# Kernel tuning notes

Measured on AMD Instinct MI355X. Metric: run time of the kernel, lower is better.

The kernel has to match this reference:

```python
import math
import jax, jax.numpy as jnp
import numpy as np

T, D, H = 2048, 2048, 16
C = D // H
EPS = 1e-6


def _rope_tables(c, t):
    inv_freq = 1.0 / (10000.0 ** (jnp.arange(0, c, 2, dtype=jnp.float32) / c))
    freqs = jnp.arange(t, dtype=jnp.float32)[:, None] * inv_freq[None, :]  # (T, C/2)
    return jnp.sin(freqs), jnp.cos(freqs)


def _rotate_every_two(x):
    x1 = x[..., ::2]
    x2 = x[..., 1::2]
    return jnp.stack((-x2, x1), axis=-1).reshape(x.shape)


def _apply_rope(x_htc, sin, cos):
    # sin/cos: (T, C/2) -> repeat each freq twice along channel -> (1, T, C)
    sin = jnp.repeat(sin, 2, axis=-1)[None]
    cos = jnp.repeat(cos, 2, axis=-1)[None]
    return x_htc * cos + _rotate_every_two(x_htc) * sin


def _layernorm(x, w):
    mu = jnp.mean(x, axis=-1, keepdims=True)
    var = jnp.var(x, axis=-1, keepdims=True)
    return (x - mu) / jnp.sqrt(var + EPS) * w


def setup_inputs() -> dict:
    key = jax.random.key(0)
    ks = jax.random.split(key, 4)
    x = jax.random.normal(ks[0], (T, D), dtype=jnp.float32)
    W_attn = jax.random.normal(ks[1], (3 * D, D), dtype=jnp.float32) * 0.02
    b_attn = jnp.zeros((3 * D,), dtype=jnp.float32)
    W_proj = jax.random.normal(ks[2], (D, D), dtype=jnp.float32) * 0.02
    b_proj = jnp.zeros((D,), dtype=jnp.float32)
    q_ln_w = jnp.ones((C,), dtype=jnp.float32)
    k_ln_w = jnp.ones((C,), dtype=jnp.float32)
    return {"x": x, "W_attn": W_attn, "b_attn": b_attn, "W_proj": W_proj,
            "b_proj": b_proj, "q_ln_w": q_ln_w, "k_ln_w": k_ln_w}


def reference(x, W_attn, b_attn, W_proj, b_proj, q_ln_w, k_ln_w):
    t, d = x.shape
    qkv = x @ W_attn.T + b_attn                      # (T, 3D)
    q, k, v = jnp.split(qkv, 3, axis=-1)
    q = q.reshape(t, H, C).transpose(1, 0, 2)        # (H, T, C)
    k = k.reshape(t, H, C).transpose(1, 0, 2)
    v = v.reshape(t, H, C).transpose(1, 0, 2)
    q = _layernorm(q, q_ln_w)
    k = _layernorm(k, k_ln_w)
    sin, cos = _rope_tables(C, t)
    q = _apply_rope(q, sin, cos)
    k = _apply_rope(k, sin, cos)
    a = jnp.einsum("htc,hsc->hts", q, k)             # (H, T, T)
    causal = jnp.tril(jnp.ones((1, t, t))) == 0
    a = jnp.where(causal, float("-inf"), a)
    scaling = math.sqrt(C)                            # q_ln active
    a = jax.nn.softmax(a.astype(jnp.float32) / scaling, axis=-1).astype(x.dtype)
    out = jnp.einsum("hts,hsc->htc", a, v)           # (H, T, C)
    out = out.transpose(1, 0, 2).reshape(t, d)       # (T, D)
    return out @ W_proj.T + b_proj
```

## Files before the change

### kernel.cpp

```cpp
#include <hip/hip_runtime.h>
#include <hip/hip_bf16.h>
#include <math.h>

#define T_DIM 2048
#define D_DIM 2048
#define H_DIM 16
#define C_DIM 128

typedef __bf16 bf16;
typedef __attribute__((ext_vector_type(8))) __bf16 bf16x8;
typedef __attribute__((ext_vector_type(4))) __bf16 bf16x4;
typedef __attribute__((ext_vector_type(2))) __bf16 bf16x2;
typedef __attribute__((ext_vector_type(4))) float f32x4;

__device__ __forceinline__ void gload_lds16(const void* g, void* l) {
  __builtin_amdgcn_global_load_lds((__attribute__((address_space(1))) void*)g,
                                   (__attribute__((address_space(3))) void*)l,
                                   16, 0, 0);
}

__global__ __launch_bounds__(256) void cvt3(
    const float* __restrict__ x, const float* __restrict__ wa, const float* __restrict__ wp,
    bf16* __restrict__ xo, bf16* __restrict__ wao, bf16* __restrict__ wpo)
{
  const int NX = 1048576, NA = 3145728;
  int i = blockIdx.x * 256 + threadIdx.x;
  for (; i < 5242880; i += 2048 * 256) {
    const float* s; bf16* d; int off;
    if (i < NX)            { s = x;  d = xo;  off = i; }
    else if (i < NX + NA)  { s = wa; d = wao; off = i - NX; }
    else                   { s = wp; d = wpo; off = i - NX - NA; }
    float4 v = reinterpret_cast<const float4*>(s)[off];
    bf16x4 o;
    o[0] = (bf16)v.x; o[1] = (bf16)v.y; o[2] = (bf16)v.z; o[3] = (bf16)v.w;
    reinterpret_cast<bf16x4*>(d)[off] = o;
  }
}

__global__ __launch_bounds__(512, 2) void gemm384_bt_bias(
    const bf16* __restrict__ A, const bf16* __restrict__ B,
    const float* __restrict__ bias, float* __restrict__ C,
    int M, int N, int K)
{
  __shared__ __align__(16) bf16 Asl[2][128 * 64];
  __shared__ __align__(16) bf16 Bsl[2][384 * 64];
  const int tid = threadIdx.x;
  const int lane = tid & 63;
  const int wv = tid >> 6;
  const int g = lane >> 4, r16 = lane & 15;
  const int wm4 = wv >> 1;
  const int wn2 = wv & 1;

  int bid = blockIdx.x;
  int bid2 = (bid & 7) * 32 + (bid >> 3);
  const int ntn = N / 384;
  const int bn = bid2 % ntn, bm = bid2 / ntn;

  const size_t Abase = (size_t)(bm * 128) * K;
  const size_t Bbase = (size_t)(bn * 384) * K;

  f32x4 acc[4][2][3] = {};
  bf16x8 a[2][2], b[3][2];

  auto stageA = [&](int bb, int t) {
#pragma unroll
    for (int i = 0; i < 2; ++i) {
      int c = i * 512 + tid;
      int r = c >> 3, p = c & 7, j = p ^ (r & 7);
      gload_lds16(A + Abase + (size_t)r * K + t * 64 + j * 8,
                  (char*)&Asl[bb][0] + (size_t)c * 16);
    }
  };
  auto stageB = [&](int bb, int u, int t) {
#pragma unroll
    for (int i = 0; i < 2; ++i) {
      int c = i * 512 + tid;
      int r = c >> 3, p = c & 7, j = p ^ (r & 7);
      gload_lds16(B + Bbase + (size_t)(u * 128 + r) * K + t * 64 + j * 8,
                  (char*)&Bsl[bb][0] + u * 16384 + (size_t)c * 16);
    }
  };
  auto readA = [&](int bufi) {
#pragma unroll
    for (int R = 0; R < 2; ++R) {
      int ar = wm4 * 32 + R * 16 + r16;
#pragma unroll
      for (int ks = 0; ks < 2; ++ks)
        a[R][ks] = *reinterpret_cast<const bf16x8*>(
            &Asl[bufi][ar * 64 + (((ks * 4 + g) ^ (ar & 7)) << 3)]);
    }
  };
  auto readB = [&](int bufi, int q) {
#pragma unroll
    for (int F = 0; F < 3; ++F) {
      int br = q * 96 + wn2 * 48 + F * 16 + r16;
#pragma unroll
      for (int ks = 0; ks < 2; ++ks)
        b[F][ks] = *reinterpret_cast<const bf16x8*>(
            &Bsl[bufi][br * 64 + (((ks * 4 + g) ^ (br & 7)) << 3)]);
    }
  };
  auto mfma12 = [&](f32x4 (&cq)[2][3]) {
    __builtin_amdgcn_s_setprio(1);
#pragma unroll
    for (int ks = 0; ks < 2; ++ks)
#pragma unroll
      for (int R = 0; R < 2; ++R)
#pragma unroll
        for (int F = 0; F < 3; ++F)
          cq[R][F] = __builtin_amdgcn_mfma_f32_16x16x32_bf16(a[R][ks], b[F][ks], cq[R][F], 0, 0, 0);
    __builtin_amdgcn_s_setprio(0);
  };

#define VMSYNC(VM)                                                \
  asm volatile("s_waitcnt vmcnt(" #VM ")" ::: "memory");          \
  __builtin_amdgcn_s_barrier();                                   \
  asm volatile("s_waitcnt lgkmcnt(0)" ::: "memory");              \
  __builtin_amdgcn_sched_barrier(0);
#define BARSYNC()                                                 \
  __builtin_amdgcn_s_barrier();                                   \
  asm volatile("s_waitcnt lgkmcnt(0)" ::: "memory");              \
  __builtin_amdgcn_sched_barrier(0);

  stageA(0, 0); stageB(0, 0, 0); stageB(0, 1, 0); stageB(0, 2, 0);
  asm volatile("s_waitcnt vmcnt(4)" ::: "memory");
  __builtin_amdgcn_s_barrier();

  const int NT = K >> 6;
  for (int t = 0; t < NT; ++t) {
    const int cb = t & 1, nb = cb ^ 1;
    const bool pf = (t + 1 < NT);
    readA(cb);
    readB(cb, 0);
    if (pf) stageA(nb, t + 1);
    VMSYNC(4)
    mfma12(acc[0]);
    __builtin_amdgcn_s_barrier();
    readB(cb, 1);
    if (pf) stageB(nb, 0, t + 1);
    VMSYNC(4)
    mfma12(acc[1]);
    __builtin_amdgcn_s_barrier();
    readB(cb, 2);
    if (pf) stageB(nb, 1, t + 1);
    BARSYNC()
    mfma12(acc[2]);
    __builtin_amdgcn_s_barrier();
    readB(cb, 3);
    if (pf) stageB(nb, 2, t + 1);
    VMSYNC(4)
    mfma12(acc[3]);
    __builtin_amdgcn_s_barrier();
  }
#undef VMSYNC
#undef BARSYNC

#pragma unroll
  for (int q = 0; q < 4; ++q)
#pragma unroll
    for (int R = 0; R < 2; ++R)
#pragma unroll
      for (int F = 0; F < 3; ++F) {
        int row0 = bm * 128 + wm4 * 32 + R * 16 + g * 4;
        int col  = bn * 384 + q * 96 + wn2 * 48 + F * 16 + r16;
        float bv = bias[col];
#pragma unroll
        for (int rr = 0; rr < 4; ++rr)
          C[(size_t)(row0 + rr) * N + col] = acc[q][R][F][rr] + bv;
      }
}

__global__ __launch_bounds__(256) void gemm_bt_bias(
    const bf16* __restrict__ A, const bf16* __restrict__ B,
    const float* __restrict__ bias, float* __restrict__ C,
    int M, int N, int K)
{
  __shared__ __align__(16) bf16 As[2][128 * 32];
  __shared__ __align__(16) bf16 Bs[2][128 * 32];
  const int tid = threadIdx.x;
  const int lane = tid & 63;
  const int w = tid >> 6;
  const int wm = (w >> 1) * 64, wn = (w & 1) * 64;
  const int g = lane >> 4;
  const int r16 = lane & 15;
  const int bm = blockIdx.y, bn = blockIdx.x;

  f32x4 acc[4][4] = {};

  const size_t Abase = (size_t)(bm * 128) * K;
  const size_t Bbase = (size_t)(bn * 128) * K;

  auto stage = [&](int bb, int k0) {
#pragma unroll
    for (int c = 0; c < 2; ++c) {
      int e = c * 256 + tid;
      int row = e >> 2, col = (e & 3) * 8;
      gload_lds16(A + Abase + (size_t)row * K + k0 + col, (char*)&As[bb][0] + (size_t)e * 16);
      gload_lds16(B + Bbase + (size_t)row * K + k0 + col, (char*)&Bs[bb][0] + (size_t)e * 16);
    }
  };

  stage(0, 0);
  __syncthreads();

  for (int k0 = 0; k0 < K; k0 += 32) {
    const int cur = (k0 >> 5) & 1;
    if (k0 + 32 < K) stage(cur ^ 1, k0 + 32);
    bf16x8 a[4], b[4];
#pragma unroll
    for (int m = 0; m < 4; ++m)
      a[m] = *reinterpret_cast<const bf16x8*>(&As[cur][(wm + m * 16 + r16) * 32 + g * 8]);
#pragma unroll
    for (int n = 0; n < 4; ++n)
      b[n] = *reinterpret_cast<const bf16x8*>(&Bs[cur][(wn + n * 16 + r16) * 32 + g * 8]);
    __builtin_amdgcn_s_setprio(1);
#pragma unroll
    for (int m = 0; m < 4; ++m)
#pragma unroll
      for (int n = 0; n < 4; ++n)
        acc[m][n] = __builtin_amdgcn_mfma_f32_16x16x32_bf16(a[m], b[n], acc[m][n], 0, 0, 0);
    __builtin_amdgcn_s_setprio(0);
    __syncthreads();
  }

#pragma unroll
  for (int m = 0; m < 4; ++m) {
    int row0 = bm * 128 + wm + m * 16 + g * 4;
#pragma unroll
    for (int n = 0; n < 4; ++n) {
      int col = bn * 128 + wn + n * 16 + r16;
      float bv = bias[col];
#pragma unroll
      for (int rr = 0; rr < 4; ++rr)
        C[(size_t)(row0 + rr) * N + col] = acc[m][n][rr] + bv;
    }
  }
}

__global__ __launch_bounds__(256) void lnrope_vt_kernel(
    const float* __restrict__ qkv, const float* __restrict__ qw,
    const float* __restrict__ kw, bf16* __restrict__ qo, bf16* __restrict__ ko,
    bf16* __restrict__ vt)
{
  __shared__ bf16 tile[32][33];
  const int tid = threadIdx.x;
  if (blockIdx.x < 8192) {
    const int lane = tid & 63;
    const int wid = blockIdx.x * 4 + (tid >> 6);
    const int h = wid >> 11;
    const int t = wid & (T_DIM - 1);
    const int c0 = lane * 2;

    float inv_freq = exp2f(-13.287712379549449f * (float)c0 * (1.0f / 128.0f));
    float fr = (float)t * inv_freq;
    float sn = sinf(fr), cs = cosf(fr);
    const float scaleq = 0.08838834764831845f;

#pragma unroll
    for (int which = 0; which < 2; ++which) {
      const float* base = qkv + (size_t)t * (3 * D_DIM) + which * D_DIM + h * C_DIM;
      float2 v = *reinterpret_cast<const float2*>(base + c0);
      float s = v.x + v.y;
#pragma unroll
      for (int m = 32; m; m >>= 1) s += __shfl_xor(s, m);
      float mu = s * (1.0f / 128.0f);
      float d0 = v.x - mu, d1 = v.y - mu;
      float ss = d0 * d0 + d1 * d1;
#pragma unroll
      for (int m = 32; m; m >>= 1) ss += __shfl_xor(ss, m);
      float rstd = rsqrtf(ss * (1.0f / 128.0f) + 1e-6f);
      const float* wgt = which ? kw : qw;
      float x0 = d0 * rstd * wgt[c0], x1 = d1 * rstd * wgt[c0 + 1];
      float o0 = x0 * cs - x1 * sn;
      float o1 = x1 * cs + x0 * sn;
      if (!which) { o0 *= scaleq; o1 *= scaleq; }
      bf16* out = (which ? ko : qo) + ((size_t)h * T_DIM + t) * C_DIM + c0;
      bf16x2 ob; ob[0] = (bf16)o0; ob[1] = (bf16)o1;
      *reinterpret_cast<bf16x2*>(out) = ob;
    }
  } else {
    const int vb = blockIdx.x - 8192;
    const int t0 = (vb & 63) * 32;
    const int c0 = ((vb >> 6) & 3) * 32;
    const int h = vb >> 8;
    const int tx = tid & 31, ty = tid >> 5;
#pragma unroll
    for (int i = 0; i < 4; ++i) {
      int t = t0 + ty + i * 8;
      tile[ty + i * 8][tx] =
          (bf16)qkv[(size_t)t * (3 * D_DIM) + 2 * D_DIM + h * C_DIM + c0 + tx];
    }
    __syncthreads();
#pragma unroll
    for (int i = 0; i < 4; ++i) {
      int c = c0 + ty + i * 8;
      vt[((size_t)h * C_DIM + c) * T_DIM + t0 + tx] = tile[tx][ty + i * 8];
    }
  }
}

__global__ __launch_bounds__(256, 4) void attn_kernel(
    const bf16* __restrict__ Q, const bf16* __restrict__ K,
    const bf16* __restrict__ VT, bf16* __restrict__ AO,
    float* __restrict__ U, float* __restrict__ ML)
{
  __shared__ __align__(16) bf16 Ks[2][32 * 128];
  __shared__ __align__(16) bf16 Vs[2][128 * 32];
  __shared__ __align__(16) bf16 p_lds[4][16 * 32];
  const int tid = threadIdx.x;
  const int lane = tid & 63;
  const int w = tid >> 6;
  const int g = lane >> 4, r16 = lane & 15;
  const int h = blockIdx.y;
  const int b = blockIdx.x;

  int qb, kb0, kb1, sp;
  if (b < 32) { qb = 16 + (b >> 1); sp = b & 1; kb0 = sp * 32; kb1 = sp ? (2 * qb + 2) : 32; }
  else        { qb = 47 - b;        sp = -1;    kb0 = 0;       kb1 = 2 * qb + 2; }
  const int qr0 = qb * 64 + w * 16;
  const int qrow = qr0 + r16;

  const bf16* Qh = Q + (size_t)h * T_DIM * C_DIM;
  const bf16* Kh = K + (size_t)h * T_DIM * C_DIM;
  const bf16* Vh = VT + (size_t)h * C_DIM * T_DIM;

  bf16x8 qf[4];
#pragma unroll
  for (int kk = 0; kk < 4; ++kk)
    qf[kk] = *reinterpret_cast<const bf16x8*>(
        &Qh[(size_t)qrow * C_DIM + kk * 32 + g * 8]);

  float mrow = -INFINITY, lrow = 0.f;
  f32x4 o[8] = {};

  auto stage = [&](int bb, int kb) {
    const bf16* Kt = Kh + (size_t)(kb * 32) * C_DIM;
    const bf16* Vt = Vh + kb * 32;
#pragma unroll
    for (int i = 0; i < 2; ++i) {
      int e = i * 256 + tid;
      int r = e >> 4, p = e & 15, j = p ^ (r & 7);
      gload_lds16(Kt + r * C_DIM + j * 8, (char*)&Ks[bb][0] + (size_t)e * 16);
    }
#pragma unroll
    for (int i = 0; i < 2; ++i) {
      int e = i * 256 + tid;
      int r = e >> 2, p = e & 3, j = p ^ ((r >> 1) & 3);
      gload_lds16(Vt + (size_t)r * T_DIM + j * 8, (char*)&Vs[bb][0] + (size_t)e * 16);
    }
  };

  stage(0, kb0);
  __syncthreads();
  int buf = 0;

  for (int kb = kb0; kb < kb1; ++kb) {
    if (kb + 1 < kb1) stage(buf ^ 1, kb + 1);

    f32x4 sacc[2] = {};
    __builtin_amdgcn_s_setprio(1);
#pragma unroll
    for (int n = 0; n < 2; ++n) {
      int kr = n * 16 + r16;
      const bf16* kbase = &Ks[buf][kr << 7];
#pragma unroll
      for (int kk = 0; kk < 4; ++kk) {
        bf16x8 kf = *reinterpret_cast<const bf16x8*>(
            kbase + (((kk * 4 + g) ^ (kr & 7)) << 3));
        sacc[n] = __builtin_amdgcn_mfma_f32_16x16x32_bf16(kf, qf[kk], sacc[n], 0, 0, 0);
      }
    }
    __builtin_amdgcn_s_setprio(0);
    if (kb * 32 + 31 > qr0) {
#pragma unroll
      for (int n = 0; n < 2; ++n)
#pragma unroll
        for (int rr = 0; rr < 4; ++rr)
          if (kb * 32 + n * 16 + g * 4 + rr > qrow) sacc[n][rr] = -3.0e38f;
    }
    float mx = fmaxf(fmaxf(fmaxf(sacc[0][0], sacc[0][1]), fmaxf(sacc[0][2], sacc[0][3])),
                     fmaxf(fmaxf(sacc[1][0], sacc[1][1]), fmaxf(sacc[1][2], sacc[1][3])));
    mx = fmaxf(mx, __shfl_xor(mx, 16));
    mx = fmaxf(mx, __shfl_xor(mx, 32));
    float alpha = 1.0f;
    bool need = __any(mx > mrow + 8.0f);
    if (need) {
      float mnew = fmaxf(mrow, mx);
      alpha = __expf(mrow - mnew);
      mrow = mnew;
    }
    float ps = 0.f;
#pragma unroll
    for (int n = 0; n < 2; ++n)
#pragma unroll
      for (int rr = 0; rr < 4; ++rr) {
        float p = __expf(sacc[n][rr] - mrow);
        sacc[n][rr] = p;
        ps += p;
      }
    ps += __shfl_xor(ps, 16);
    ps += __shfl_xor(ps, 32);
    lrow = lrow * alpha + ps;
    if (need) {
#pragma unroll
      for (int nc = 0; nc < 8; ++nc)
#pragma unroll
        for (int rr = 0; rr < 4; ++rr)
          o[nc][rr] *= alpha;
    }
    {
      bf16* prow = &p_lds[w][r16 << 5];
      const int ssw = (r16 >> 1) & 3;
#pragma unroll
      for (int n = 0; n < 2; ++n) {
        bf16x4 pk;
        pk[0] = (bf16)sacc[n][0]; pk[1] = (bf16)sacc[n][1];
        pk[2] = (bf16)sacc[n][2]; pk[3] = (bf16)sacc[n][3];
        int c8 = 2 * n + (g >> 1);
        *reinterpret_cast<bf16x4*>(prow + (((c8 ^ ssw) << 3) | ((g & 1) << 2))) = pk;
      }
    }
    asm volatile("s_waitcnt lgkmcnt(0)" ::: "memory");
    __builtin_amdgcn_s_setprio(1);
    bf16x8 pf = *reinterpret_cast<const bf16x8*>(
        &p_lds[w][(r16 << 5) + ((g ^ ((r16 >> 1) & 3)) << 3)]);
#pragma unroll
    for (int nc = 0; nc < 8; ++nc) {
      int vr = nc * 16 + r16;
      bf16x8 vf = *reinterpret_cast<const bf16x8*>(
          &Vs[buf][(vr << 5) + ((g ^ ((vr >> 1) & 3)) << 3)]);
      o[nc] = __builtin_amdgcn_mfma_f32_16x16x32_bf16(vf, pf, o[nc], 0, 0, 0);
    }
    __builtin_amdgcn_s_setprio(0);
    __syncthreads();
    buf ^= 1;
  }

  if (sp < 0) {
    float inv = 1.0f / lrow;
    bf16* arow = &AO[(size_t)qrow * D_DIM + h * C_DIM + (g << 2)];
#pragma unroll
    for (int nc = 0; nc < 8; ++nc) {
      bf16x4 ob;
      ob[0] = (bf16)(o[nc][0] * inv); ob[1] = (bf16)(o[nc][1] * inv);
      ob[2] = (bf16)(o[nc][2] * inv); ob[3] = (bf16)(o[nc][3] * inv);
      *reinterpret_cast<bf16x4*>(arow + nc * 16) = ob;
    }
  } else {
    const int qi = qb - 16;
    const size_t ubase = ((size_t)(h * 16 + qi) * 2 + sp) * (64 * 128);
    const size_t mlbase = (size_t)(h * 16 + qi) * 256 + sp * 128;
    const int row = w * 16 + r16;
    float* urow = &U[ubase + (size_t)row * 128 + (g << 2)];
#pragma unroll
    for (int nc = 0; nc < 8; ++nc)
      *reinterpret_cast<f32x4*>(urow + nc * 16) = o[nc];
    if (g == 0) {
      ML[mlbase + row] = mrow;
      ML[mlbase + 64 + row] = lrow;
    }
  }
}

__global__ __launch_bounds__(256) void attn_combine(
    const float* __restrict__ U, const float* __restrict__ ML, bf16* __restrict__ AO)
{
  int idx = blockIdx.x * 256 + threadIdx.x;
  int c4 = (idx & 31) * 4;
  int r = idx >> 5;
  int trow = r & 63;
  int qi = (r >> 6) & 15;
  int h = r >> 10;

  size_t mlbase = (size_t)(h * 16 + qi) * 256;
  float m0 = ML[mlbase + trow],       l0 = ML[mlbase + 64 + trow];
  float m1 = ML[mlbase + 128 + trow], l1 = ML[mlbase + 192 + trow];
  float m = fmaxf(m0, m1);
  float a0 = __expf(m0 - m), a1 = __expf(m1 - m);
  float inv = 1.0f / (l0 * a0 + l1 * a1);

  size_t t0 = ((size_t)(h * 16 + qi) * 2) * (64 * 128) + (size_t)trow * 128 + c4;
  float4 u0 = *reinterpret_cast<const float4*>(U + t0);
  float4 u1 = *reinterpret_cast<const float4*>(U + t0 + 64 * 128);
  int t = 1024 + qi * 64 + trow;
  bf16x4 ob;
  ob[0] = (bf16)((u0.x * a0 + u1.x * a1) * inv);
  ob[1] = (bf16)((u0.y * a0 + u1.y * a1) * inv);
  ob[2] = (bf16)((u0.z * a0 + u1.z * a1) * inv);
  ob[3] = (bf16)((u0.w * a0 + u1.w * a1) * inv);
  *reinterpret_cast<bf16x4*>(&AO[(size_t)t * D_DIM + h * C_DIM + c4]) = ob;
}

extern "C" void kernel_launch(void* const* d_in, const int* in_sizes, int n_in,
                              void* d_out, int out_size, void* d_ws, size_t ws_size,
                              hipStream_t stream)
{
  const float* x      = (const float*)d_in[0];
  const float* W_attn = (const float*)d_in[1];
  const float* b_attn = (const float*)d_in[2];
  const float* W_proj = (const float*)d_in[3];
  const float* b_proj = (const float*)d_in[4];
  const float* q_ln_w = (const float*)d_in[5];
  const float* k_ln_w = (const float*)d_in[6];

  char* ws = (char*)d_ws;
  bf16*  x_bf  = (bf16*)(ws + 0);
  bf16*  wa_bf = (bf16*)(ws + 8388608);
  bf16*  wp_bf = (bf16*)(ws + 33554432);
  float* qkv   = (float*)(ws + 41943040);
  bf16*  q_bf  = (bf16*)(ws + 92274688);
  bf16*  k_bf  = (bf16*)(ws + 100663296);
  bf16*  vt    = (bf16*)(ws + 109051904);
  bf16*  ao    = (bf16*)(ws + 117440512);
  float* U  = (float*)(ws + 41943040);
  float* ML = (float*)(ws + 58720256);

  cvt3<<<2048, 256, 0, stream>>>(x, W_attn, W_proj, x_bf, wa_bf, wp_bf);

  gemm384_bt_bias<<<dim3((T_DIM / 128) * (3 * D_DIM / 384)), dim3(512), 0, stream>>>(
      x_bf, wa_bf, b_attn, qkv, T_DIM, 3 * D_DIM, D_DIM);

  lnrope_vt_kernel<<<8192 + 4096, 256, 0, stream>>>(qkv, q_ln_w, k_ln_w, q_bf, k_bf, vt);

  attn_kernel<<<dim3(48, H_DIM), 256, 0, stream>>>(q_bf, k_bf, vt, ao, U, ML);
  attn_combine<<<2048, 256, 0, stream>>>(U, ML, ao);

  gemm_bt_bias<<<dim3(D_DIM / 128, T_DIM / 128), 256, 0, stream>>>(
      ao, wp_bf, b_proj, (float*)d_out, T_DIM, D_DIM, D_DIM);
}
```

Baseline: 191.3 us.

## Remap QKV GEMM warps to 2x4 grid with register-reused A/B fragments

Changes the wave layout of the 128x384 QKV GEMM from 4x2 (32 rows each, cycling over four B column groups) to 2x4 (64 rows by 96 columns per wave). Each wave now holds two A and two B fragment sets and runs four MFMA phases over their cross products, so the LDS fragment reads per K-step drop from 4 A plus 12 B loads to 2 A plus 2 B groups. Global prefetch is regrouped into three phases with a single vmcnt(0) wait at the end of each iteration. This raises register use and gives up the finer-grained vmcnt overlap of the previous schedule.

```diff
diff --git a/kernel.cpp b/kernel.cpp
--- a/kernel.cpp
+++ b/kernel.cpp
@@ -48,8 +48,8 @@
   const int lane = tid & 63;
   const int wv = tid >> 6;
   const int g = lane >> 4, r16 = lane & 15;
-  const int wm4 = wv >> 1;
-  const int wn2 = wv & 1;
+  const int wm = wv >> 2;
+  const int wn = wv & 3;
 
   int bid = blockIdx.x;
   int bid2 = (bid & 7) * 32 + (bid >> 3);
@@ -59,8 +59,9 @@
   const size_t Abase = (size_t)(bm * 128) * K;
   const size_t Bbase = (size_t)(bn * 384) * K;
 
-  f32x4 acc[4][2][3] = {};
-  bf16x8 a[2][2], b[3][2];
+  f32x4 acc[2][2][2][3] = {};
+  bf16x8 a0[2][2], a1[2][2];
+  bf16x8 b0[3][2], b1[3][2];
 
   auto stageA = [&](int bb, int t) {
 #pragma unroll
@@ -80,27 +81,27 @@
                   (char*)&Bsl[bb][0] + u * 16384 + (size_t)c * 16);
     }
   };
-  auto readA = [&](int bufi) {
+  auto readAh = [&](bf16x8 (&dst)[2][2], int bufi, int qr) {
 #pragma unroll
     for (int R = 0; R < 2; ++R) {
-      int ar = wm4 * 32 + R * 16 + r16;
+      int ar = wm * 64 + qr * 32 + R * 16 + r16;
 #pragma unroll
       for (int ks = 0; ks < 2; ++ks)
-        a[R][ks] = *reinterpret_cast<const bf16x8*>(
+        dst[R][ks] = *reinterpret_cast<const bf16x8*>(
             &Asl[bufi][ar * 64 + (((ks * 4 + g) ^ (ar & 7)) << 3)]);
     }
   };
-  auto readB = [&](int bufi, int q) {
+  auto readBh = [&](bf16x8 (&dst)[3][2], int bufi, int qc) {
 #pragma unroll
     for (int F = 0; F < 3; ++F) {
-      int br = q * 96 + wn2 * 48 + F * 16 + r16;
+      int br = wn * 96 + qc * 48 + F * 16 + r16;
 #pragma unroll
       for (int ks = 0; ks < 2; ++ks)
-        b[F][ks] = *reinterpret_cast<const bf16x8*>(
+        dst[F][ks] = *reinterpret_cast<const bf16x8*>(
             &Bsl[bufi][br * 64 + (((ks * 4 + g) ^ (br & 7)) << 3)]);
     }
   };
-  auto mfma12 = [&](f32x4 (&cq)[2][3]) {
+  auto mfma12 = [&](f32x4 (&cq)[2][3], bf16x8 (&aa)[2][2], bf16x8 (&bb)[3][2]) {
     __builtin_amdgcn_s_setprio(1);
 #pragma unroll
     for (int ks = 0; ks < 2; ++ks)
@@ -108,66 +109,60 @@
       for (int R = 0; R < 2; ++R)
 #pragma unroll
         for (int F = 0; F < 3; ++F)
-          cq[R][F] = __builtin_amdgcn_mfma_f32_16x16x32_bf16(a[R][ks], b[F][ks], cq[R][F], 0, 0, 0);
+          cq[R][F] = __builtin_amdgcn_mfma_f32_16x16x32_bf16(aa[R][ks], bb[F][ks], cq[R][F], 0, 0, 0);
     __builtin_amdgcn_s_setprio(0);
   };
 
-#define VMSYNC(VM)                                                \
-  asm volatile("s_waitcnt vmcnt(" #VM ")" ::: "memory");          \
+#define PHASESYNC()                                               \
   __builtin_amdgcn_s_barrier();                                   \
   asm volatile("s_waitcnt lgkmcnt(0)" ::: "memory");              \
   __builtin_amdgcn_sched_barrier(0);
-#define BARSYNC()                                                 \
-  __builtin_amdgcn_s_barrier();                                   \
-  asm volatile("s_waitcnt lgkmcnt(0)" ::: "memory");              \
-  __builtin_amdgcn_sched_barrier(0);
 
   stageA(0, 0); stageB(0, 0, 0); stageB(0, 1, 0); stageB(0, 2, 0);
-  asm volatile("s_waitcnt vmcnt(4)" ::: "memory");
+  asm volatile("s_waitcnt vmcnt(0)" ::: "memory");
   __builtin_amdgcn_s_barrier();
 
   const int NT = K >> 6;
   for (int t = 0; t < NT; ++t) {
     const int cb = t & 1, nb = cb ^ 1;
     const bool pf = (t + 1 < NT);
-    readA(cb);
-    readB(cb, 0);
-    if (pf) stageA(nb, t + 1);
-    VMSYNC(4)
-    mfma12(acc[0]);
+    readAh(a0, cb, 0);
+    readBh(b0, cb, 0);
+    if (pf) { stageA(nb, t + 1); stageB(nb, 0, t + 1); }
+    PHASESYNC()
+    mfma12(acc[0][0], a0, b0);
     __builtin_amdgcn_s_barrier();
-    readB(cb, 1);
-    if (pf) stageB(nb, 0, t + 1);
-    VMSYNC(4)
-    mfma12(acc[1]);
+    readBh(b1, cb, 1);
+    if (pf) stageB(nb, 1, t + 1);
+    PHASESYNC()
+    mfma12(acc[0][1], a0, b1);
     __builtin_amdgcn_s_barrier();
-    readB(cb, 2);
-    if (pf) stageB(nb, 1, t + 1);
-    BARSYNC()
-    mfma12(acc[2]);
+    readAh(a1, cb, 1);
+    if (pf) stageB(nb, 2, t + 1);
+    PHASESYNC()
+    mfma12(acc[1][1], a1, b1);
     __builtin_amdgcn_s_barrier();
-    readB(cb, 3);
-    if (pf) stageB(nb, 2, t + 1);
-    VMSYNC(4)
-    mfma12(acc[3]);
+    mfma12(acc[1][0], a1, b0);
+    asm volatile("s_waitcnt vmcnt(0)" ::: "memory");
     __builtin_amdgcn_s_barrier();
   }
-#undef VMSYNC
-#undef BARSYNC
-
-#pragma unroll
-  for (int q = 0; q < 4; ++q)
-#pragma unroll
-    for (int R = 0; R < 2; ++R)
-#pragma unroll
-      for (int F = 0; F < 3; ++F) {
-        int row0 = bm * 128 + wm4 * 32 + R * 16 + g * 4;
-        int col  = bn * 384 + q * 96 + wn2 * 48 + F * 16 + r16;
-        float bv = bias[col];
-#pragma unroll
-        for (int rr = 0; rr < 4; ++rr)
-          C[(size_t)(row0 + rr) * N + col] = acc[q][R][F][rr] + bv;
-      }
+#undef PHASESYNC
+
+#pragma unroll
+  for (int qr = 0; qr < 2; ++qr)
+#pragma unroll
+    for (int qc = 0; qc < 2; ++qc)
+#pragma unroll
+      for (int R = 0; R < 2; ++R)
+#pragma unroll
+        for (int F = 0; F < 3; ++F) {
+          int row0 = bm * 128 + wm * 64 + qr * 32 + R * 16 + g * 4;
+          int col  = bn * 384 + wn * 96 + qc * 48 + F * 16 + r16;
+          float bv = bias[col];
+#pragma unroll
+          for (int rr = 0; rr < 4; ++rr)
+            C[(size_t)(row0 + rr) * N + col] = acc[qr][qc][R][F][rr] + bv;
+        }
 }
 
 __global__ __launch_bounds__(256) void gemm_bt_bias(
```

Result: no change. 187.7 us (-1.9%).
